# Optimization experiments

Measured on AMD Instinct MI355X. Metric: run time of the kernel, lower is better.

The kernel has to match this reference:

```python
import jax, jax.numpy as jnp
import numpy as np

FORGET_BIAS = 1.0


def _lstm(x, W, b, reverse):
    """BasicLSTMCell scan. x: [B,T,F], W: [F+U, 4U], b: [4U]. Returns [B,T,U]."""
    B = x.shape[0]
    U = W.shape[1] // 4

    def step(carry, xt):
        c, h = carry
        z = jnp.concatenate([xt, h], axis=-1) @ W + b  # [B, 4U]
        i, j, f, o = jnp.split(z, 4, axis=-1)  # TF BasicLSTMCell gate order
        c_new = c * jax.nn.sigmoid(f + FORGET_BIAS) + jax.nn.sigmoid(i) * jnp.tanh(j)
        h_new = jax.nn.sigmoid(o) * jnp.tanh(c_new)
        return (c_new, h_new), h_new

    xs = jnp.swapaxes(x, 0, 1)  # [T,B,F]
    init = (jnp.zeros((B, U), x.dtype), jnp.zeros((B, U), x.dtype))
    _, hs = jax.lax.scan(step, init, xs, reverse=reverse)  # outputs aligned to input time
    return jnp.swapaxes(hs, 0, 1)  # [B,T,U]


def setup_inputs() -> dict:
    key = jax.random.key(0)
    k1, k2, k3 = jax.random.split(key, 3)
    B, T, F, U = 64, 2048, 128, 128
    scale = 1.0 / np.sqrt(F + U)
    x = jax.random.normal(k1, (B, T, F), dtype=jnp.float32)
    W_fw = jax.random.normal(k2, (F + U, 4 * U), dtype=jnp.float32) * scale
    W_bw = jax.random.normal(k3, (F + U, 4 * U), dtype=jnp.float32) * scale
    b_fw = jnp.zeros((4 * U,), dtype=jnp.float32)
    b_bw = jnp.zeros((4 * U,), dtype=jnp.float32)
    return {"x": x, "W_fw": W_fw, "b_fw": b_fw, "W_bw": W_bw, "b_bw": b_bw}


def reference(x, W_fw, b_fw, W_bw, b_bw):
    out_fw = _lstm(x, W_fw, b_fw, reverse=False)  # [B,T,U]
    out_bw = _lstm(x, W_bw, b_bw, reverse=True)   # [B,T,U], time-aligned with input
    return jnp.concatenate([out_fw, out_bw], axis=2)  # [B,T,2U]
```

## Files before the change

kernel.cpp:

```cpp
#include <hip/hip_runtime.h>
#include <hip/hip_bf16.h>


typedef _Float16 half8_t __attribute__((ext_vector_type(8)));
typedef _Float16 half4_t __attribute__((ext_vector_type(4)));
typedef float floatx4 __attribute__((ext_vector_type(4)));

#define T_SEQ 2048
#define GDIM 512
#define KLOG2E 1.4426950408889634f

__device__ __forceinline__ float exp2_f(float x) {
#if __has_builtin(__builtin_amdgcn_exp2f)
    return __builtin_amdgcn_exp2f(x);
#else
    return __expf(x * 0.6931471805599453f);
#endif
}
__device__ __forceinline__ float sigm2(float x) {
    return __builtin_amdgcn_rcpf(1.0f + exp2_f(x));
}
__device__ __forceinline__ float tanh2(float x) {
    return 1.0f - 2.0f * __builtin_amdgcn_rcpf(1.0f + exp2_f(x));
}
__device__ __forceinline__ float sel4(floatx4 v, int m) {
    float a = (m & 1) ? v[1] : v[0];
    float b = (m & 1) ? v[3] : v[2];
    return (m & 2) ? b : a;
}

__global__ __launch_bounds__(256) void zx_gemm(
    const float* __restrict__ x,
    const float* __restrict__ Wfw, const float* __restrict__ bfw,
    const float* __restrict__ Wbw, const float* __restrict__ bbw,
    _Float16* __restrict__ zx) {
    const int tid = threadIdx.x;
    const int tt = blockIdx.x;
    const int b = blockIdx.y;
    const int d = blockIdx.z;
    const int t0 = tt * 64;
    const float* W = d ? Wbw : Wfw;
    const float* bias = d ? bbw : bfw;
    const int bg = b >> 2, m = b & 3;

    __shared__ _Float16 lA[64 * 136];
    __shared__ _Float16 lB[128 * 136];

    const float* xp = x + ((size_t)b * T_SEQ + t0) * 128;
    for (int i = 0; i < 8; ++i) {
        int v = i * 256 + tid;
        int r = v >> 5;
        int kq = (v & 31) << 2;
        float4 f = *(const float4*)(xp + r * 128 + kq);
        half4_t h4;
        h4[0] = (_Float16)f.x; h4[1] = (_Float16)f.y;
        h4[2] = (_Float16)f.z; h4[3] = (_Float16)f.w;
        *(half4_t*)&lA[r * 136 + kq] = h4;
    }

    const int w1 = tid >> 6, lane = tid & 63, lm = lane & 15, q = lane >> 4;

    for (int ct = 0; ct < 4; ++ct) {
        const float* wp = W + ct * 128;
        for (int i = 0; i < 16; ++i) {
            int v = i * 256 + tid;
            int k = v >> 5;
            int cq = (v & 31) << 2;
            float4 f = *(const float4*)(wp + (size_t)k * GDIM + cq);
            lB[(cq + 0) * 136 + k] = (_Float16)f.x;
            lB[(cq + 1) * 136 + k] = (_Float16)f.y;
            lB[(cq + 2) * 136 + k] = (_Float16)f.z;
            lB[(cq + 3) * 136 + k] = (_Float16)f.w;
        }
        __syncthreads();

        floatx4 acc[8];
#pragma unroll
        for (int nt = 0; nt < 8; ++nt) acc[nt] = (floatx4){0.f, 0.f, 0.f, 0.f};
#pragma unroll
        for (int ks = 0; ks < 4; ++ks) {
            const int k0 = ks * 32 + q * 8;
            half8_t a = *(const half8_t*)&lA[(w1 * 16 + lm) * 136 + k0];
#pragma unroll
            for (int nt = 0; nt < 8; ++nt) {
                half8_t bf = *(const half8_t*)&lB[(nt * 16 + lm) * 136 + k0];
                acc[nt] = __builtin_amdgcn_mfma_f32_16x16x32_f16(a, bf, acc[nt], 0, 0, 0);
            }
        }
        const float sc = (ct == 1) ? (2.0f * KLOG2E) : (-KLOG2E);
        const float badd = (ct == 2) ? 1.0f : 0.0f;
#pragma unroll
        for (int nt = 0; nt < 8; ++nt) {
            float bv = bias[ct * 128 + nt * 16 + lm] + badd;
#pragma unroll
            for (int rr = 0; rr < 4; ++rr) {
                int t = t0 + w1 * 16 + q * 4 + rr;
                size_t oi = (((size_t)(d * 16 + bg) * T_SEQ + t) * 4 + ct) * 512
                            + nt * 64 + m * 16 + lm;
                zx[oi] = (_Float16)(sc * (acc[nt][rr] + bv));
            }
        }
        __syncthreads();
    }
}

__global__ __launch_bounds__(512) void lstm_rec(
    const float* __restrict__ Wfw, const float* __restrict__ Wbw,
    const _Float16* __restrict__ zx, float* __restrict__ out) {
    const int bg = blockIdx.x;
    const int d = blockIdx.y;
    const int b0 = bg * 4;
    const float* Wd = d ? Wbw : Wfw;
    const int tid = threadIdx.x;
    const int w = tid >> 6, lane = tid & 63, lm = lane & 15, q = lane >> 4;
    const int m = q;
    const int u = w * 16 + lm;

    __shared__ _Float16 hbuf[2][4 * 144];

    half8_t bfr[4][4];
#pragma unroll
    for (int g = 0; g < 4; ++g) {
        const float sc = (g == 1) ? (2.0f * KLOG2E) : (-KLOG2E);
#pragma unroll
        for (int ks = 0; ks < 4; ++ks) {
            int col = g * 128 + u;
            int kb = 128 + ks * 32 + q * 8;
            half8_t f;
#pragma unroll
            for (int j = 0; j < 8; ++j)
                f[j] = (_Float16)(sc * Wd[(size_t)(kb + j) * GDIM + col]);
            bfr[g][ks] = f;
        }
    }

    for (int i = tid; i < 2 * 4 * 144; i += 512) ((_Float16*)hbuf)[i] = (_Float16)0.f;

    const _Float16* zx_d = zx + (size_t)(d * 16 + bg) * T_SEQ * 2048;
    const unsigned zoff = (unsigned)(w * 64 + lane);
    const unsigned obase = (unsigned)((b0 + m) * T_SEQ) * 256u + (unsigned)(d * 128 + u);

    _Float16 na[4], nb[4];
    {
        const _Float16* r0 = zx_d + (size_t)(d ? (T_SEQ - 1) : 0) * 2048;
        const _Float16* r1 = zx_d + (size_t)(d ? (T_SEQ - 2) : 1) * 2048;
#pragma unroll
        for (int g = 0; g < 4; ++g) na[g] = r0[zoff + g * 512];
#pragma unroll
        for (int g = 0; g < 4; ++g) nb[g] = r1[zoff + g * 512];
    }
    float cst = 0.f;
    __syncthreads();

#define REC_STEP(RD, WR, NREG, SCUR)                                          \
    {                                                                         \
        const int t_ = d ? (T_SEQ - 1 - (SCUR)) : (SCUR);                     \
        half8_t af[4];                                                        \
        _Pragma("unroll")                                                     \
        for (int ks = 0; ks < 4; ++ks)                                        \
            af[ks] = *(const half8_t*)&hbuf[RD][(lm & 3) * 144 + ks * 32 + q * 8]; \
        float zc[4];                                                          \
        _Pragma("unroll")                                                     \
        for (int g = 0; g < 4; ++g) zc[g] = (float)NREG[g];                   \
        int sn_ = (SCUR) + 2; if (sn_ > T_SEQ - 1) sn_ = T_SEQ - 1;           \
        const int tn_ = d ? (T_SEQ - 1 - sn_) : sn_;                          \
        const _Float16* zrow_ = zx_d + (size_t)tn_ * 2048;                    \
        _Pragma("unroll")                                                     \
        for (int g = 0; g < 4; ++g) NREG[g] = zrow_[zoff + g * 512];          \
        floatx4 acg[4];                                                       \
        _Pragma("unroll")                                                     \
        for (int g = 0; g < 4; ++g) acg[g] = (floatx4){0.f, 0.f, 0.f, 0.f};   \
        _Pragma("unroll")                                                     \
        for (int ks = 0; ks < 4; ++ks)                                        \
            _Pragma("unroll")                                                 \
            for (int g = 0; g < 4; ++g)                                       \
                acg[g] = __builtin_amdgcn_mfma_f32_16x16x32_f16(af[ks], bfr[g][ks], acg[g], 0, 0, 0); \
        float zi = sel4(acg[0], m) + zc[0];                                   \
        float zj = sel4(acg[1], m) + zc[1];                                   \
        float zf = sel4(acg[2], m) + zc[2];                                   \
        float zo = sel4(acg[3], m) + zc[3];                                   \
        cst = cst * sigm2(zf) + sigm2(zi) * tanh2(zj);                        \
        float hv = sigm2(zo) * tanh2(2.0f * KLOG2E * cst);                    \
        hbuf[WR][m * 144 + u] = (_Float16)hv;                                 \
        float* orow_ = out + (size_t)t_ * 256;                                \
        orow_[obase] = hv;                                                    \
        __builtin_amdgcn_sched_barrier(0);                                    \
        asm volatile("s_waitcnt lgkmcnt(0)");                                 \
        __builtin_amdgcn_s_barrier();                                         \
        __builtin_amdgcn_sched_barrier(0);                                    \
    }

    for (int s = 0; s < T_SEQ; s += 2) {
        REC_STEP(0, 1, na, s);
        REC_STEP(1, 0, nb, s + 1);
    }
#undef REC_STEP
}

extern "C" void kernel_launch(void* const* d_in, const int* in_sizes, int n_in,
                              void* d_out, int out_size, void* d_ws, size_t ws_size,
                              hipStream_t stream) {
    const float* x   = (const float*)d_in[0];
    const float* Wfw = (const float*)d_in[1];
    const float* bfw = (const float*)d_in[2];
    const float* Wbw = (const float*)d_in[3];
    const float* bbw = (const float*)d_in[4];
    float* out = (float*)d_out;
    _Float16* zx = (_Float16*)d_ws;

    dim3 g1(32, 64, 2);
    zx_gemm<<<g1, 256, 0, stream>>>(x, Wfw, bfw, Wbw, bbw, zx);
    dim3 g2(16, 2);
    lstm_rec<<<g2, 512, 0, stream>>>(Wfw, Wbw, zx, out);
}
```

Baseline: 1.445 ms.

## Merge both LSTM directions into one block with two column tiles per wave

Both directions now run in a single 512-thread block, four waves per direction, and each wave computes two 16-unit column tiles instead of one. The grid shrinks from 32 blocks to 16. The precomputed input projection is now loaded straight into the MFMA accumulator, which removes the separate add after the matmul. In exchange, each wave does twice the MFMA and gate work per step, the two directions share one barrier, and the per-thread recurrent weight fragments double. Together with launch_bounds(512,2), that risks exceeding the register budget and spilling.

```diff
diff --git a/kernel.cpp b/kernel.cpp
--- a/kernel.cpp
+++ b/kernel.cpp
@@ -104,52 +104,58 @@
     }
 }
 
-__global__ __launch_bounds__(512) void lstm_rec(
+__global__ __launch_bounds__(512, 2) void lstm_rec(
     const float* __restrict__ Wfw, const float* __restrict__ Wbw,
     const _Float16* __restrict__ zx, float* __restrict__ out) {
     const int bg = blockIdx.x;
-    const int d = blockIdx.y;
     const int b0 = bg * 4;
+    const int tid = threadIdx.x;
+    const int w8 = tid >> 6;
+    const int d = w8 >> 2;
+    const int wd = w8 & 3;
+    const int lane = tid & 63, lm = lane & 15, q = lane >> 4;
     const float* Wd = d ? Wbw : Wfw;
-    const int tid = threadIdx.x;
-    const int w = tid >> 6, lane = tid & 63, lm = lane & 15, q = lane >> 4;
-    const int m = q;
-    const int u = w * 16 + lm;
-
-    __shared__ _Float16 hbuf[2][4 * 144];
-
-    half8_t bfr[4][4];
+
+    __shared__ _Float16 hbuf[2][2][4 * 144];
+
+    half8_t bfr[4][2][4];
 #pragma unroll
     for (int g = 0; g < 4; ++g) {
         const float sc = (g == 1) ? (2.0f * KLOG2E) : (-KLOG2E);
 #pragma unroll
-        for (int ks = 0; ks < 4; ++ks) {
-            int col = g * 128 + u;
-            int kb = 128 + ks * 32 + q * 8;
-            half8_t f;
-#pragma unroll
-            for (int j = 0; j < 8; ++j)
-                f[j] = (_Float16)(sc * Wd[(size_t)(kb + j) * GDIM + col]);
-            bfr[g][ks] = f;
-        }
-    }
-
-    for (int i = tid; i < 2 * 4 * 144; i += 512) ((_Float16*)hbuf)[i] = (_Float16)0.f;
+        for (int c = 0; c < 2; ++c)
+#pragma unroll
+            for (int ks = 0; ks < 4; ++ks) {
+                int col = g * 128 + wd * 32 + c * 16 + lm;
+                int kb = 128 + ks * 32 + q * 8;
+                half8_t f;
+#pragma unroll
+                for (int j = 0; j < 8; ++j)
+                    f[j] = (_Float16)(sc * Wd[(size_t)(kb + j) * GDIM + col]);
+                bfr[g][c][ks] = f;
+            }
+    }
+
+    for (int i = tid; i < 2 * 2 * 4 * 144; i += 512) ((_Float16*)hbuf)[i] = (_Float16)0.f;
 
     const _Float16* zx_d = zx + (size_t)(d * 16 + bg) * T_SEQ * 2048;
-    const unsigned zoff = (unsigned)(w * 64 + lane);
-    const unsigned obase = (unsigned)((b0 + m) * T_SEQ) * 256u + (unsigned)(d * 128 + u);
-
-    _Float16 na[4], nb[4];
+    const unsigned zoff = (unsigned)(wd * 128 + lane);
+    const unsigned obase = (unsigned)((b0 + q) * T_SEQ) * 256u
+                           + (unsigned)(d * 128 + wd * 32 + lm);
+
+    _Float16 na[8], nb[8];
     {
         const _Float16* r0 = zx_d + (size_t)(d ? (T_SEQ - 1) : 0) * 2048;
         const _Float16* r1 = zx_d + (size_t)(d ? (T_SEQ - 2) : 1) * 2048;
 #pragma unroll
-        for (int g = 0; g < 4; ++g) na[g] = r0[zoff + g * 512];
-#pragma unroll
-        for (int g = 0; g < 4; ++g) nb[g] = r1[zoff + g * 512];
-    }
-    float cst = 0.f;
+        for (int g = 0; g < 4; ++g)
+#pragma unroll
+            for (int c = 0; c < 2; ++c) {
+                na[g * 2 + c] = r0[zoff + g * 512 + c * 64];
+                nb[g * 2 + c] = r1[zoff + g * 512 + c * 64];
+            }
+    }
+    float cst0 = 0.f, cst1 = 0.f;
     __syncthreads();
 
 #define REC_STEP(RD, WR, NREG, SCUR)                                          \
@@ -158,32 +164,46 @@
         half8_t af[4];                                                        \
         _Pragma("unroll")                                                     \
         for (int ks = 0; ks < 4; ++ks)                                        \
-            af[ks] = *(const half8_t*)&hbuf[RD][(lm & 3) * 144 + ks * 32 + q * 8]; \
-        float zc[4];                                                          \
-        _Pragma("unroll")                                                     \
-        for (int g = 0; g < 4; ++g) zc[g] = (float)NREG[g];                   \
+            af[ks] = *(const half8_t*)&hbuf[d][RD][(lm & 3) * 144 + ks * 32 + q * 8]; \
+        float zc[8];                                                          \
+        _Pragma("unroll")                                                     \
+        for (int i = 0; i < 8; ++i) zc[i] = (float)NREG[i];                   \
         int sn_ = (SCUR) + 2; if (sn_ > T_SEQ - 1) sn_ = T_SEQ - 1;           \
         const int tn_ = d ? (T_SEQ - 1 - sn_) : sn_;                          \
         const _Float16* zrow_ = zx_d + (size_t)tn_ * 2048;                    \
         _Pragma("unroll")                                                     \
-        for (int g = 0; g < 4; ++g) NREG[g] = zrow_[zoff + g * 512];          \
-        floatx4 acg[4];                                                       \
-        _Pragma("unroll")                                                     \
-        for (int g = 0; g < 4; ++g) acg[g] = (floatx4){0.f, 0.f, 0.f, 0.f};   \
+        for (int g = 0; g < 4; ++g)                                           \
+            _Pragma("unroll")                                                 \
+            for (int c = 0; c < 2; ++c)                                       \
+                NREG[g * 2 + c] = zrow_[zoff + g * 512 + c * 64];             \
+        floatx4 acg[4][2];                                                    \
+        _Pragma("unroll")                                                     \
+        for (int g = 0; g < 4; ++g)                                           \
+            _Pragma("unroll")                                                 \
+            for (int c = 0; c < 2; ++c) {                                     \
+                float v_ = zc[g * 2 + c];                                     \
+                acg[g][c] = (floatx4){v_, v_, v_, v_};                        \
+            }                                                                 \
         _Pragma("unroll")                                                     \
         for (int ks = 0; ks < 4; ++ks)                                        \
             _Pragma("unroll")                                                 \
-            for (int g = 0; g < 4; ++g)                                       \
-                acg[g] = __builtin_amdgcn_mfma_f32_16x16x32_f16(af[ks], bfr[g][ks], acg[g], 0, 0, 0); \
-        float zi = sel4(acg[0], m) + zc[0];                                   \
-        float zj = sel4(acg[1], m) + zc[1];                                   \
-        float zf = sel4(acg[2], m) + zc[2];                                   \
-        float zo = sel4(acg[3], m) + zc[3];                                   \
-        cst = cst * sigm2(zf) + sigm2(zi) * tanh2(zj);                        \
-        float hv = sigm2(zo) * tanh2(2.0f * KLOG2E * cst);                    \
-        hbuf[WR][m * 144 + u] = (_Float16)hv;                                 \
+            for (int g = 0; g < 4; ++g) {                                     \
+                acg[g][0] = __builtin_amdgcn_mfma_f32_16x16x32_f16(af[ks], bfr[g][0][ks], acg[g][0], 0, 0, 0); \
+                acg[g][1] = __builtin_amdgcn_mfma_f32_16x16x32_f16(af[ks], bfr[g][1][ks], acg[g][1], 0, 0, 0); \
+            }                                                                 \
+        float zi0 = sel4(acg[0][0], q), zi1 = sel4(acg[0][1], q);             \
+        float zj0 = sel4(acg[1][0], q), zj1 = sel4(acg[1][1], q);             \
+        float zf0 = sel4(acg[2][0], q), zf1 = sel4(acg[2][1], q);             \
+        float zo0 = sel4(acg[3][0], q), zo1 = sel4(acg[3][1], q);             \
+        cst0 = cst0 * sigm2(zf0) + sigm2(zi0) * tanh2(zj0);                   \
+        cst1 = cst1 * sigm2(zf1) + sigm2(zi1) * tanh2(zj1);                   \
+        float h0_ = sigm2(zo0) * tanh2(2.0f * KLOG2E * cst0);                 \
+        float h1_ = sigm2(zo1) * tanh2(2.0f * KLOG2E * cst1);                 \
+        hbuf[d][WR][q * 144 + wd * 32 + lm] = (_Float16)h0_;                  \
+        hbuf[d][WR][q * 144 + wd * 32 + 16 + lm] = (_Float16)h1_;             \
         float* orow_ = out + (size_t)t_ * 256;                                \
-        orow_[obase] = hv;                                                    \
+        orow_[obase] = h0_;                                                   \
+        orow_[obase + 16] = h1_;                                              \
         __builtin_amdgcn_sched_barrier(0);                                    \
         asm volatile("s_waitcnt lgkmcnt(0)");                                 \
         __builtin_amdgcn_s_barrier();                                         \
@@ -210,6 +230,6 @@
 
     dim3 g1(32, 64, 2);
     zx_gemm<<<g1, 256, 0, stream>>>(x, Wfw, bfw, Wbw, bbw, zx);
-    dim3 g2(16, 2);
+    dim3 g2(16, 1);
     lstm_rec<<<g2, 512, 0, stream>>>(Wfw, Wbw, zx, out);
 }
```

New measurement: 2.242 ms. +55.2%, slower.

## Restructure input-projection GEMM to keep weights in registers and prefetch x tiles

Applied to the files above, without the earlier changes.

The zx GEMM now launches one block per (gate chunk, batch, direction). Each block loads its scaled fp16 weight fragments into registers once and streams 16 time tiles of x through them, double-buffering the global loads of the next tile. This removes the repeated LDS staging of W and the transposed shared-memory writes, and folds the scale and bias into the weights and accumulator init. In exchange it launches far fewer blocks (512) and uses many registers per thread.

```diff
diff --git a/kernel.cpp b/kernel.cpp
--- a/kernel.cpp
+++ b/kernel.cpp
@@ -3,7 +3,6 @@
 
 
 typedef _Float16 half8_t __attribute__((ext_vector_type(8)));
-typedef _Float16 half4_t __attribute__((ext_vector_type(4)));
 typedef float floatx4 __attribute__((ext_vector_type(4)));
 
 #define T_SEQ 2048
@@ -29,79 +28,94 @@
     return (m & 2) ? b : a;
 }
 
-__global__ __launch_bounds__(256) void zx_gemm(
+__global__ __launch_bounds__(512, 2) void zx_gemm2(
     const float* __restrict__ x,
     const float* __restrict__ Wfw, const float* __restrict__ bfw,
     const float* __restrict__ Wbw, const float* __restrict__ bbw,
     _Float16* __restrict__ zx) {
-    const int tid = threadIdx.x;
-    const int tt = blockIdx.x;
+    const int ct = blockIdx.x;
     const int b = blockIdx.y;
     const int d = blockIdx.z;
-    const int t0 = tt * 64;
     const float* W = d ? Wbw : Wfw;
     const float* bias = d ? bbw : bfw;
     const int bg = b >> 2, m = b & 3;
-
-    __shared__ _Float16 lA[64 * 136];
-    __shared__ _Float16 lB[128 * 136];
-
-    const float* xp = x + ((size_t)b * T_SEQ + t0) * 128;
-    for (int i = 0; i < 8; ++i) {
-        int v = i * 256 + tid;
-        int r = v >> 5;
-        int kq = (v & 31) << 2;
-        float4 f = *(const float4*)(xp + r * 128 + kq);
-        half4_t h4;
-        h4[0] = (_Float16)f.x; h4[1] = (_Float16)f.y;
-        h4[2] = (_Float16)f.z; h4[3] = (_Float16)f.w;
-        *(half4_t*)&lA[r * 136 + kq] = h4;
-    }
-
-    const int w1 = tid >> 6, lane = tid & 63, lm = lane & 15, q = lane >> 4;
-
-    for (int ct = 0; ct < 4; ++ct) {
-        const float* wp = W + ct * 128;
-        for (int i = 0; i < 16; ++i) {
-            int v = i * 256 + tid;
-            int k = v >> 5;
-            int cq = (v & 31) << 2;
-            float4 f = *(const float4*)(wp + (size_t)k * GDIM + cq);
-            lB[(cq + 0) * 136 + k] = (_Float16)f.x;
-            lB[(cq + 1) * 136 + k] = (_Float16)f.y;
-            lB[(cq + 2) * 136 + k] = (_Float16)f.z;
-            lB[(cq + 3) * 136 + k] = (_Float16)f.w;
+    const int tid = threadIdx.x;
+    const int w = tid >> 6, lane = tid & 63, lm = lane & 15, q = lane >> 4;
+    const float sc = (ct == 1) ? (2.0f * KLOG2E) : (-KLOG2E);
+    const float badd = (ct == 2) ? 1.0f : 0.0f;
+
+    half8_t bfr[8][4];
+#pragma unroll
+    for (int fc = 0; fc < 8; ++fc)
+#pragma unroll
+        for (int ks = 0; ks < 4; ++ks) {
+            const int col = ct * 128 + fc * 16 + lm;
+            const int kb = ks * 32 + q * 8;
+            half8_t f;
+#pragma unroll
+            for (int j = 0; j < 8; ++j)
+                f[j] = (_Float16)(sc * W[(size_t)(kb + j) * GDIM + col]);
+            bfr[fc][ks] = f;
         }
-        __syncthreads();
-
-        floatx4 acc[8];
-#pragma unroll
-        for (int nt = 0; nt < 8; ++nt) acc[nt] = (floatx4){0.f, 0.f, 0.f, 0.f};
-#pragma unroll
-        for (int ks = 0; ks < 4; ++ks) {
-            const int k0 = ks * 32 + q * 8;
-            half8_t a = *(const half8_t*)&lA[(w1 * 16 + lm) * 136 + k0];
-#pragma unroll
-            for (int nt = 0; nt < 8; ++nt) {
-                half8_t bf = *(const half8_t*)&lB[(nt * 16 + lm) * 136 + k0];
-                acc[nt] = __builtin_amdgcn_mfma_f32_16x16x32_f16(a, bf, acc[nt], 0, 0, 0);
-            }
-        }
-        const float sc = (ct == 1) ? (2.0f * KLOG2E) : (-KLOG2E);
-        const float badd = (ct == 2) ? 1.0f : 0.0f;
-#pragma unroll
-        for (int nt = 0; nt < 8; ++nt) {
-            float bv = bias[ct * 128 + nt * 16 + lm] + badd;
-#pragma unroll
-            for (int rr = 0; rr < 4; ++rr) {
-                int t = t0 + w1 * 16 + q * 4 + rr;
-                size_t oi = (((size_t)(d * 16 + bg) * T_SEQ + t) * 4 + ct) * 512
-                            + nt * 64 + m * 16 + lm;
-                zx[oi] = (_Float16)(sc * (acc[nt][rr] + bv));
-            }
-        }
-        __syncthreads();
-    }
+    float sb[8];
+#pragma unroll
+    for (int fc = 0; fc < 8; ++fc)
+        sb[fc] = sc * (bias[ct * 128 + fc * 16 + lm] + badd);
+
+    const float* xp = x + ((size_t)b * T_SEQ + w * 16 + lm) * 128 + q * 8;
+    _Float16* zb = zx + (((size_t)(d * 16 + bg) * T_SEQ + w * 16 + q * 4) * 4 + ct) * 512
+                   + m * 16 + lm;
+
+    float4 pa[8], pb[8];
+#pragma unroll
+    for (int ks = 0; ks < 4; ++ks) {
+        pa[ks * 2]     = *(const float4*)(xp + ks * 32);
+        pa[ks * 2 + 1] = *(const float4*)(xp + ks * 32 + 4);
+    }
+
+#define ZX_TILE(CUR, NXT, TT)                                                 \
+    {                                                                         \
+        if ((TT) < 15) {                                                      \
+            const float* xn_ = xp + (size_t)((TT) + 1) * 128 * 128;           \
+            _Pragma("unroll")                                                 \
+            for (int ks = 0; ks < 4; ++ks) {                                  \
+                NXT[ks * 2]     = *(const float4*)(xn_ + ks * 32);            \
+                NXT[ks * 2 + 1] = *(const float4*)(xn_ + ks * 32 + 4);        \
+            }                                                                 \
+        }                                                                     \
+        half8_t af[4];                                                        \
+        _Pragma("unroll")                                                     \
+        for (int ks = 0; ks < 4; ++ks) {                                      \
+            float4 a_ = CUR[ks * 2], b_ = CUR[ks * 2 + 1];                    \
+            half8_t f_;                                                       \
+            f_[0] = (_Float16)a_.x; f_[1] = (_Float16)a_.y;                   \
+            f_[2] = (_Float16)a_.z; f_[3] = (_Float16)a_.w;                   \
+            f_[4] = (_Float16)b_.x; f_[5] = (_Float16)b_.y;                   \
+            f_[6] = (_Float16)b_.z; f_[7] = (_Float16)b_.w;                   \
+            af[ks] = f_;                                                      \
+        }                                                                     \
+        floatx4 acc[8];                                                       \
+        _Pragma("unroll")                                                     \
+        for (int fc = 0; fc < 8; ++fc)                                        \
+            acc[fc] = (floatx4){sb[fc], sb[fc], sb[fc], sb[fc]};              \
+        _Pragma("unroll")                                                     \
+        for (int ks = 0; ks < 4; ++ks)                                        \
+            _Pragma("unroll")                                                 \
+            for (int fc = 0; fc < 8; ++fc)                                    \
+                acc[fc] = __builtin_amdgcn_mfma_f32_16x16x32_f16(af[ks], bfr[fc][ks], acc[fc], 0, 0, 0); \
+        _Float16* zr_ = zb + (size_t)(TT) * 128 * 4 * 512;                    \
+        _Pragma("unroll")                                                     \
+        for (int fc = 0; fc < 8; ++fc)                                        \
+            _Pragma("unroll")                                                 \
+            for (int rr = 0; rr < 4; ++rr)                                    \
+                zr_[(size_t)rr * 2048 + fc * 64] = (_Float16)acc[fc][rr];     \
+    }
+
+    for (int tt = 0; tt < 16; tt += 2) {
+        ZX_TILE(pa, pb, tt);
+        ZX_TILE(pb, pa, tt + 1);
+    }
+#undef ZX_TILE
 }
 
 __global__ __launch_bounds__(512) void lstm_rec(
@@ -208,8 +222,8 @@
     float* out = (float*)d_out;
     _Float16* zx = (_Float16*)d_ws;
 
-    dim3 g1(32, 64, 2);
-    zx_gemm<<<g1, 256, 0, stream>>>(x, Wfw, bfw, Wbw, bbw, zx);
+    dim3 g1(4, 64, 2);
+    zx_gemm2<<<g1, 512, 0, stream>>>(x, Wfw, bfw, Wbw, bbw, zx);
     dim3 g2(16, 2);
     lstm_rec<<<g2, 512, 0, stream>>>(Wfw, Wbw, zx, out);
 }
```

Result: no change. 1.455 ms (+0.7%).

## Fuse input projection into recurrent LSTM kernel, computing x·W every four steps

Applied to the files above, without the earlier changes.

Removes the separate zx_gemm kernel and the fp16 zx workspace round trip. The recurrent kernel now loads x directly, converts it to fp16 and computes the input projection with MFMA once per four time steps, four rows of the tile covering four consecutive steps. It also holds both the input and recurrent weight fragments in registers. This saves one kernel launch and the global write and read of the projected gates. The cost is extra MFMA work and more register pressure on the serial critical path, which runs on only 32 blocks.

```diff
diff --git a/kernel.cpp b/kernel.cpp
--- a/kernel.cpp
+++ b/kernel.cpp
@@ -3,7 +3,6 @@
 
 
 typedef _Float16 half8_t __attribute__((ext_vector_type(8)));
-typedef _Float16 half4_t __attribute__((ext_vector_type(4)));
 typedef float floatx4 __attribute__((ext_vector_type(4)));
 
 #define T_SEQ 2048
@@ -29,144 +28,70 @@
     return (m & 2) ? b : a;
 }
 
-__global__ __launch_bounds__(256) void zx_gemm(
+__global__ __launch_bounds__(512, 2) void lstm_fused(
     const float* __restrict__ x,
     const float* __restrict__ Wfw, const float* __restrict__ bfw,
     const float* __restrict__ Wbw, const float* __restrict__ bbw,
-    _Float16* __restrict__ zx) {
-    const int tid = threadIdx.x;
-    const int tt = blockIdx.x;
-    const int b = blockIdx.y;
-    const int d = blockIdx.z;
-    const int t0 = tt * 64;
-    const float* W = d ? Wbw : Wfw;
-    const float* bias = d ? bbw : bfw;
-    const int bg = b >> 2, m = b & 3;
-
-    __shared__ _Float16 lA[64 * 136];
-    __shared__ _Float16 lB[128 * 136];
-
-    const float* xp = x + ((size_t)b * T_SEQ + t0) * 128;
-    for (int i = 0; i < 8; ++i) {
-        int v = i * 256 + tid;
-        int r = v >> 5;
-        int kq = (v & 31) << 2;
-        float4 f = *(const float4*)(xp + r * 128 + kq);
-        half4_t h4;
-        h4[0] = (_Float16)f.x; h4[1] = (_Float16)f.y;
-        h4[2] = (_Float16)f.z; h4[3] = (_Float16)f.w;
-        *(half4_t*)&lA[r * 136 + kq] = h4;
-    }
-
-    const int w1 = tid >> 6, lane = tid & 63, lm = lane & 15, q = lane >> 4;
-
-    for (int ct = 0; ct < 4; ++ct) {
-        const float* wp = W + ct * 128;
-        for (int i = 0; i < 16; ++i) {
-            int v = i * 256 + tid;
-            int k = v >> 5;
-            int cq = (v & 31) << 2;
-            float4 f = *(const float4*)(wp + (size_t)k * GDIM + cq);
-            lB[(cq + 0) * 136 + k] = (_Float16)f.x;
-            lB[(cq + 1) * 136 + k] = (_Float16)f.y;
-            lB[(cq + 2) * 136 + k] = (_Float16)f.z;
-            lB[(cq + 3) * 136 + k] = (_Float16)f.w;
-        }
-        __syncthreads();
-
-        floatx4 acc[8];
-#pragma unroll
-        for (int nt = 0; nt < 8; ++nt) acc[nt] = (floatx4){0.f, 0.f, 0.f, 0.f};
-#pragma unroll
-        for (int ks = 0; ks < 4; ++ks) {
-            const int k0 = ks * 32 + q * 8;
-            half8_t a = *(const half8_t*)&lA[(w1 * 16 + lm) * 136 + k0];
-#pragma unroll
-            for (int nt = 0; nt < 8; ++nt) {
-                half8_t bf = *(const half8_t*)&lB[(nt * 16 + lm) * 136 + k0];
-                acc[nt] = __builtin_amdgcn_mfma_f32_16x16x32_f16(a, bf, acc[nt], 0, 0, 0);
-            }
-        }
-        const float sc = (ct == 1) ? (2.0f * KLOG2E) : (-KLOG2E);
-        const float badd = (ct == 2) ? 1.0f : 0.0f;
-#pragma unroll
-        for (int nt = 0; nt < 8; ++nt) {
-            float bv = bias[ct * 128 + nt * 16 + lm] + badd;
-#pragma unroll
-            for (int rr = 0; rr < 4; ++rr) {
-                int t = t0 + w1 * 16 + q * 4 + rr;
-                size_t oi = (((size_t)(d * 16 + bg) * T_SEQ + t) * 4 + ct) * 512
-                            + nt * 64 + m * 16 + lm;
-                zx[oi] = (_Float16)(sc * (acc[nt][rr] + bv));
-            }
-        }
-        __syncthreads();
-    }
-}
-
-__global__ __launch_bounds__(512) void lstm_rec(
-    const float* __restrict__ Wfw, const float* __restrict__ Wbw,
-    const _Float16* __restrict__ zx, float* __restrict__ out) {
+    float* __restrict__ out) {
     const int bg = blockIdx.x;
     const int d = blockIdx.y;
     const int b0 = bg * 4;
     const float* Wd = d ? Wbw : Wfw;
+    const float* bd = d ? bbw : bfw;
     const int tid = threadIdx.x;
     const int w = tid >> 6, lane = tid & 63, lm = lane & 15, q = lane >> 4;
-    const int m = q;
     const int u = w * 16 + lm;
 
     __shared__ _Float16 hbuf[2][4 * 144];
 
-    half8_t bfr[4][4];
+    half8_t bfr_x[4][4], bfr_h[4][4];
+    float sb[4];
 #pragma unroll
     for (int g = 0; g < 4; ++g) {
         const float sc = (g == 1) ? (2.0f * KLOG2E) : (-KLOG2E);
 #pragma unroll
         for (int ks = 0; ks < 4; ++ks) {
-            int col = g * 128 + u;
-            int kb = 128 + ks * 32 + q * 8;
-            half8_t f;
+            const int col = g * 128 + u;
+            const int kbx = ks * 32 + q * 8;
+            half8_t fx, fh;
 #pragma unroll
-            for (int j = 0; j < 8; ++j)
-                f[j] = (_Float16)(sc * Wd[(size_t)(kb + j) * GDIM + col]);
-            bfr[g][ks] = f;
+            for (int j = 0; j < 8; ++j) {
+                fx[j] = (_Float16)(sc * Wd[(size_t)(kbx + j) * GDIM + col]);
+                fh[j] = (_Float16)(sc * Wd[(size_t)(128 + kbx + j) * GDIM + col]);
+            }
+            bfr_x[g][ks] = fx;
+            bfr_h[g][ks] = fh;
         }
+        sb[g] = sc * (bd[g * 128 + u] + ((g == 2) ? 1.0f : 0.0f));
     }
 
     for (int i = tid; i < 2 * 4 * 144; i += 512) ((_Float16*)hbuf)[i] = (_Float16)0.f;
 
-    const _Float16* zx_d = zx + (size_t)(d * 16 + bg) * T_SEQ * 2048;
-    const unsigned zoff = (unsigned)(w * 64 + lane);
-    const unsigned obase = (unsigned)((b0 + m) * T_SEQ) * 256u + (unsigned)(d * 128 + u);
+    const int tsign = d ? -1 : 1;
+    const float* xbase = x + (size_t)(b0 + (lm >> 2)) * (T_SEQ * 128)
+                         + tsign * (lm & 3) * 128 + q * 8;
+    const unsigned obase = (unsigned)((b0 + q) * T_SEQ) * 256u
+                           + (unsigned)(d * 128 + u);
 
-    _Float16 na[4], nb[4];
+    float4 px[8];
     {
-        const _Float16* r0 = zx_d + (size_t)(d ? (T_SEQ - 1) : 0) * 2048;
-        const _Float16* r1 = zx_d + (size_t)(d ? (T_SEQ - 2) : 1) * 2048;
+        const float* xr = xbase + (size_t)(d ? (T_SEQ - 1) : 0) * 128;
 #pragma unroll
-        for (int g = 0; g < 4; ++g) na[g] = r0[zoff + g * 512];
-#pragma unroll
-        for (int g = 0; g < 4; ++g) nb[g] = r1[zoff + g * 512];
+        for (int ks = 0; ks < 4; ++ks) {
+            px[ks * 2]     = *(const float4*)(xr + ks * 32);
+            px[ks * 2 + 1] = *(const float4*)(xr + ks * 32 + 4);
+        }
     }
     float cst = 0.f;
     __syncthreads();
 
-#define REC_STEP(RD, WR, NREG, SCUR)                                          \
+#define REC_STEP(RD, WR, R, SCUR)                                             \
     {                                                                         \
         const int t_ = d ? (T_SEQ - 1 - (SCUR)) : (SCUR);                     \
         half8_t af[4];                                                        \
         _Pragma("unroll")                                                     \
         for (int ks = 0; ks < 4; ++ks)                                        \
             af[ks] = *(const half8_t*)&hbuf[RD][(lm & 3) * 144 + ks * 32 + q * 8]; \
-        float zc[4];                                                          \
-        _Pragma("unroll")                                                     \
-        for (int g = 0; g < 4; ++g) zc[g] = (float)NREG[g];                   \
-        int sn_ = (SCUR) + 2; if (sn_ > T_SEQ - 1) sn_ = T_SEQ - 1;           \
-        const int tn_ = d ? (T_SEQ - 1 - sn_) : sn_;                          \
-        const _Float16* zrow_ = zx_d + (size_t)tn_ * 2048;                    \
-        _Pragma("unroll")                                                     \
-        for (int g = 0; g < 4; ++g) NREG[g] = zrow_[zoff + g * 512];          \
         floatx4 acg[4];                                                       \
         _Pragma("unroll")                                                     \
         for (int g = 0; g < 4; ++g) acg[g] = (floatx4){0.f, 0.f, 0.f, 0.f};   \
@@ -174,25 +99,57 @@
         for (int ks = 0; ks < 4; ++ks)                                        \
             _Pragma("unroll")                                                 \
             for (int g = 0; g < 4; ++g)                                       \
-                acg[g] = __builtin_amdgcn_mfma_f32_16x16x32_f16(af[ks], bfr[g][ks], acg[g], 0, 0, 0); \
-        float zi = sel4(acg[0], m) + zc[0];                                   \
-        float zj = sel4(acg[1], m) + zc[1];                                   \
-        float zf = sel4(acg[2], m) + zc[2];                                   \
-        float zo = sel4(acg[3], m) + zc[3];                                   \
+                acg[g] = __builtin_amdgcn_mfma_f32_16x16x32_f16(af[ks], bfr_h[g][ks], acg[g], 0, 0, 0); \
+        float zi = zcs[0][R] + sel4(acg[0], q);                               \
+        float zj = zcs[1][R] + sel4(acg[1], q);                               \
+        float zf = zcs[2][R] + sel4(acg[2], q);                               \
+        float zo = zcs[3][R] + sel4(acg[3], q);                               \
         cst = cst * sigm2(zf) + sigm2(zi) * tanh2(zj);                        \
         float hv = sigm2(zo) * tanh2(2.0f * KLOG2E * cst);                    \
-        hbuf[WR][m * 144 + u] = (_Float16)hv;                                 \
-        float* orow_ = out + (size_t)t_ * 256;                                \
-        orow_[obase] = hv;                                                    \
+        hbuf[WR][q * 144 + u] = (_Float16)hv;                                 \
+        out[(size_t)t_ * 256 + obase] = hv;                                   \
         __builtin_amdgcn_sched_barrier(0);                                    \
         asm volatile("s_waitcnt lgkmcnt(0)");                                 \
         __builtin_amdgcn_s_barrier();                                         \
         __builtin_amdgcn_sched_barrier(0);                                    \
     }
 
-    for (int s = 0; s < T_SEQ; s += 2) {
-        REC_STEP(0, 1, na, s);
-        REC_STEP(1, 0, nb, s + 1);
+    floatx4 zcs[4];
+    for (int s = 0; s < T_SEQ; s += 4) {
+        half8_t axf[4];
+#pragma unroll
+        for (int ks = 0; ks < 4; ++ks) {
+            float4 a_ = px[ks * 2], b_ = px[ks * 2 + 1];
+            half8_t f_;
+            f_[0] = (_Float16)a_.x; f_[1] = (_Float16)a_.y;
+            f_[2] = (_Float16)a_.z; f_[3] = (_Float16)a_.w;
+            f_[4] = (_Float16)b_.x; f_[5] = (_Float16)b_.y;
+            f_[6] = (_Float16)b_.z; f_[7] = (_Float16)b_.w;
+            axf[ks] = f_;
+        }
+        {
+            int sn = s + 4; if (sn >= T_SEQ) sn = 0;
+            const int tbn = d ? (T_SEQ - 1 - sn) : sn;
+            const float* xr = xbase + (size_t)tbn * 128;
+#pragma unroll
+            for (int ks = 0; ks < 4; ++ks) {
+                px[ks * 2]     = *(const float4*)(xr + ks * 32);
+                px[ks * 2 + 1] = *(const float4*)(xr + ks * 32 + 4);
+            }
+        }
+#pragma unroll
+        for (int g = 0; g < 4; ++g)
+            zcs[g] = (floatx4){sb[g], sb[g], sb[g], sb[g]};
+#pragma unroll
+        for (int ks = 0; ks < 4; ++ks)
+#pragma unroll
+            for (int g = 0; g < 4; ++g)
+                zcs[g] = __builtin_amdgcn_mfma_f32_16x16x32_f16(axf[ks], bfr_x[g][ks], zcs[g], 0, 0, 0);
+
+        REC_STEP(0, 1, 0, s)
+        REC_STEP(1, 0, 1, s + 1)
+        REC_STEP(0, 1, 2, s + 2)
+        REC_STEP(1, 0, 3, s + 3)
     }
 #undef REC_STEP
 }
@@ -206,10 +163,8 @@
     const float* Wbw = (const float*)d_in[3];
     const float* bbw = (const float*)d_in[4];
     float* out = (float*)d_out;
-    _Float16* zx = (_Float16*)d_ws;
+    (void)d_ws; (void)ws_size;
 
-    dim3 g1(32, 64, 2);
-    zx_gemm<<<g1, 256, 0, stream>>>(x, Wfw, bfw, Wbw, bbw, zx);
-    dim3 g2(16, 2);
-    lstm_rec<<<g2, 512, 0, stream>>>(Wfw, Wbw, zx, out);
+    dim3 g(16, 2);
+    lstm_fused<<<g, 512, 0, stream>>>(x, Wfw, bfw, Wbw, bbw, out);
 }
```

New measurement: 1.260 ms. -12.8%, faster.
